# Performance work log

Hardware: AMD Instinct MI355X
Metric: run time of the kernel (lower is better)

## Reference

```python
import jax, jax.numpy as jnp
import numpy as np

N, F_IN, F_OUT = 8192, 512, 256


def setup_inputs() -> dict:
    key = jax.random.key(0)
    k1, k2, k3, k4 = jax.random.split(key, 4)
    x = jax.random.normal(k1, (N, F_IN), dtype=jnp.float32)
    adj = jax.random.randint(k2, (N, N), 0, 2, dtype=jnp.int32)
    # xavier_uniform with gain=1.414
    limW = 1.414 * np.sqrt(6.0 / (F_IN + F_OUT))
    W = jax.random.uniform(k3, (F_IN, F_OUT), dtype=jnp.float32, minval=-limW, maxval=limW)
    lima = 1.414 * np.sqrt(6.0 / (2 * F_OUT + 1))
    a = jax.random.uniform(k4, (2 * F_OUT, 1), dtype=jnp.float32, minval=-lima, maxval=lima)
    return {"x": x, "adj": adj, "W": W, "a": a}


def reference(x, adj, W, a):
    # h = x @ W : [N, F_out]
    h = x @ W
    f_out = h.shape[1]
    # additive score a^T [h_i ; h_j] is separable: (h @ a_l)_i + (h @ a_r)_j
    f_src = h @ a[:f_out, 0]   # [N]
    f_dst = h @ a[f_out:, 0]   # [N]
    e = jax.nn.leaky_relu(f_src[:, None] + f_dst[None, :], negative_slope=0.2)  # [N, N]
    e = jnp.where(adj > 0, e, jnp.float32(-9e15))
    attention = jax.nn.softmax(e, axis=1)  # row-wise over neighbors
    # dropout(p=0.6) is identity in eval mode
    h_prime = attention @ h  # [N, F_out]
    return h_prime
```

## Files before the change

kernel.cpp:

```cpp
#include <hip/hip_runtime.h>
#include <hip/hip_bf16.h>

#define NN 8192
#define FIN 512
#define FOUT 256
#define JTILE 64

typedef __attribute__((ext_vector_type(8))) short short8;
typedef __attribute__((ext_vector_type(4))) short short4v;
typedef __attribute__((ext_vector_type(4))) float float4v;
typedef __attribute__((ext_vector_type(16))) float float16v;

__device__ __forceinline__ short f2bf(float f) {
    union { float f; unsigned u; } v; v.f = f;
    unsigned r = (v.u + 0x7FFFu + ((v.u >> 16) & 1u)) >> 16;
    return (short)r;
}

__global__ __launch_bounds__(256) void wt_kernel(const float* __restrict__ W,
                                                 short* __restrict__ Wt) {
    __shared__ short tile[32][33];
    int tx = threadIdx.x & 31, ty = threadIdx.x >> 5;
    int k0 = blockIdx.x * 32, n0 = blockIdx.y * 32;
#pragma unroll
    for (int r = 0; r < 32; r += 8)
        tile[ty + r][tx] = f2bf(W[(size_t)(k0 + ty + r) * FOUT + n0 + tx]);
    __syncthreads();
#pragma unroll
    for (int r = 0; r < 32; r += 8)
        Wt[(size_t)(n0 + ty + r) * FIN + k0 + tx] = tile[tx][ty + r];
}

__global__ __launch_bounds__(256) void h_kernel(const float* __restrict__ x,
                                                const short* __restrict__ Wt,
                                                const float* __restrict__ a,
                                                short* __restrict__ h_t,
                                                float* __restrict__ f_src,
                                                float* __restrict__ f_dst) {
    int wave = (blockIdx.x << 2) + (threadIdx.x >> 6);
    int lane = threadIdx.x & 63;
    int m0 = (wave & 511) << 4;
    int n0 = (wave >> 9) << 6;
    int lr = lane & 15, lq = lane >> 4;

    const float* xrow = x + (size_t)(m0 + lr) * FIN + lq * 8;
    const short* wbase = Wt + (size_t)(n0 + lr) * FIN + lq * 8;

    float4v acc[4] = {};
    for (int k0 = 0; k0 < FIN; k0 += 32) {
        float4v xa = *(const float4v*)(xrow + k0);
        float4v xb = *(const float4v*)(xrow + k0 + 4);
        short8 av;
        av[0] = f2bf(xa[0]); av[1] = f2bf(xa[1]); av[2] = f2bf(xa[2]); av[3] = f2bf(xa[3]);
        av[4] = f2bf(xb[0]); av[5] = f2bf(xb[1]); av[6] = f2bf(xb[2]); av[7] = f2bf(xb[3]);
#pragma unroll
        for (int ct = 0; ct < 4; ct++) {
            short8 bv = *(const short8*)(wbase + (size_t)ct * 16 * FIN + k0);
            acc[ct] = __builtin_amdgcn_mfma_f32_16x16x32_bf16(av, bv, acc[ct], 0, 0, 0);
        }
    }
    float s_part[4] = {0.f, 0.f, 0.f, 0.f};
    float d_part[4] = {0.f, 0.f, 0.f, 0.f};
#pragma unroll
    for (int ct = 0; ct < 4; ct++) {
        int n = n0 + ct * 16 + lr;
        float al = a[n], ar = a[FOUT + n];
#pragma unroll
        for (int reg = 0; reg < 4; reg++) {
            float hv = acc[ct][reg];
            s_part[reg] = fmaf(hv, al, s_part[reg]);
            d_part[reg] = fmaf(hv, ar, d_part[reg]);
            h_t[(size_t)n * NN + (m0 + lq * 4 + reg)] = f2bf(hv);
        }
    }
#pragma unroll
    for (int off = 1; off < 16; off <<= 1) {
#pragma unroll
        for (int reg = 0; reg < 4; reg++) {
            s_part[reg] += __shfl_xor(s_part[reg], off);
            d_part[reg] += __shfl_xor(d_part[reg], off);
        }
    }
    const float LOG2E = 1.4426950408889634f;
    if (lr == 0) {
#pragma unroll
        for (int reg = 0; reg < 4; reg++) {
            atomicAdd(&f_src[m0 + lq * 4 + reg], s_part[reg] * LOG2E);
            atomicAdd(&f_dst[m0 + lq * 4 + reg], d_part[reg] * LOG2E);
        }
    }
}

__global__ __launch_bounds__(256, 2) void gat_kernel(const int* __restrict__ adj,
                                                     const short* __restrict__ h_t,
                                                     const float* __restrict__ f_src,
                                                     const float* __restrict__ f_dst,
                                                     float* __restrict__ Opart,
                                                     float* __restrict__ lpart,
                                                     int jlen) {
    __shared__ short Ht[256 * 72];
    __shared__ short Pt[64 * 72];
    __shared__ float Fd[2][64];

    const int t = threadIdx.x;
    const int i0 = blockIdx.x * 64;
    const int slice = blockIdx.y;
    const int jbase = slice * jlen;

    const int prow = t >> 2, pjq = t & 3;
    const int lane = t & 63, w = t >> 6;
    const int l31 = lane & 31, lq = lane >> 5;
    const int wn0 = w * 64;

    const float fs = f_src[i0 + prow];
    const int* adjRow = adj + (size_t)(i0 + prow) * NN;
    const short* hrow = h_t + ((size_t)t << 13);

    float16v acc00 = {}, acc01 = {}, acc10 = {}, acc11 = {};
    float lp = 0.f;

    if (t < 16) *(float4*)&Fd[0][t * 4] = *(const float4*)(f_dst + jbase + t * 4);
    int4 av0 = *(const int4*)(adjRow + jbase + pjq * 16);
    int4 av1 = *(const int4*)(adjRow + jbase + pjq * 16 + 4);
    int4 av2 = *(const int4*)(adjRow + jbase + pjq * 16 + 8);
    int4 av3 = *(const int4*)(adjRow + jbase + pjq * 16 + 12);
    __syncthreads();

    int buf = 0;
    for (int jo = 0; jo < jlen; jo += JTILE) {
        const int j0 = jbase + jo;
        {
            const float* fdc = &Fd[buf][pjq * 16];
            short8 pbl, pbh;
            int4 avs[4] = {av0, av1, av2, av3};
#pragma unroll
            for (int g = 0; g < 4; g++) {
                const int* ai = (const int*)&avs[g];
#pragma unroll
                for (int q = 0; q < 4; q++) {
                    float y = fs + fdc[g * 4 + q];
                    y = fmaxf(y, 0.2f * y);
                    float e = exp2f(y);
                    float p = (ai[q] != 0) ? e : 0.f;
                    lp += p;
                    short pb = f2bf(p);
                    if (g < 2) pbl[g * 4 + q] = pb; else pbh[(g - 2) * 4 + q] = pb;
                }
            }
            *(short8*)&Pt[prow * 72 + pjq * 16] = pbl;
            *(short8*)&Pt[prow * 72 + pjq * 16 + 8] = pbh;
        }
#pragma unroll
        for (int q = 0; q < 8; q++)
            *(short8*)&Ht[t * 72 + q * 8] = *(const short8*)(hrow + j0 + q * 8);

        if (jo + JTILE < jlen) {
            if (t < 16) *(float4*)&Fd[buf ^ 1][t * 4] = *(const float4*)(f_dst + j0 + JTILE + t * 4);
            av0 = *(const int4*)(adjRow + j0 + JTILE + pjq * 16);
            av1 = *(const int4*)(adjRow + j0 + JTILE + pjq * 16 + 4);
            av2 = *(const int4*)(adjRow + j0 + JTILE + pjq * 16 + 8);
            av3 = *(const int4*)(adjRow + j0 + JTILE + pjq * 16 + 12);
        }
        __syncthreads();

#pragma unroll
        for (int kk = 0; kk < 4; kk++) {
            short8 a0 = *(const short8*)&Pt[l31 * 72 + kk * 16 + lq * 8];
            short8 a1 = *(const short8*)&Pt[(32 + l31) * 72 + kk * 16 + lq * 8];
            short8 b0 = *(const short8*)&Ht[(wn0 + l31) * 72 + kk * 16 + lq * 8];
            short8 b1 = *(const short8*)&Ht[(wn0 + 32 + l31) * 72 + kk * 16 + lq * 8];
            acc00 = __builtin_amdgcn_mfma_f32_32x32x16_bf16(a0, b0, acc00, 0, 0, 0);
            acc01 = __builtin_amdgcn_mfma_f32_32x32x16_bf16(a0, b1, acc01, 0, 0, 0);
            acc10 = __builtin_amdgcn_mfma_f32_32x32x16_bf16(a1, b0, acc10, 0, 0, 0);
            acc11 = __builtin_amdgcn_mfma_f32_32x32x16_bf16(a1, b1, acc11, 0, 0, 0);
        }
        buf ^= 1;
        __syncthreads();
    }

    lp += __shfl_xor(lp, 1);
    lp += __shfl_xor(lp, 2);
    if (pjq == 0) lpart[slice * NN + i0 + prow] = lp;

    float* obase = Opart + ((size_t)slice * NN + i0) * FOUT;
#pragma unroll
    for (int rt = 0; rt < 2; rt++) {
#pragma unroll
        for (int nt = 0; nt < 2; nt++) {
            const float16v& av = rt == 0 ? (nt == 0 ? acc00 : acc01) : (nt == 0 ? acc10 : acc11);
#pragma unroll
            for (int reg = 0; reg < 16; reg++) {
                int row = rt * 32 + (reg & 3) + 8 * (reg >> 2) + 4 * lq;
                int n = wn0 + nt * 32 + l31;
                obase[(size_t)row * FOUT + n] = av[reg];
            }
        }
    }
}

__global__ __launch_bounds__(256) void combine_kernel(const float* __restrict__ Opart,
                                                      const float* __restrict__ lpart,
                                                      float* __restrict__ out, int slices) {
    int i = blockIdx.x, n = threadIdx.x;
    float o = 0.f, l = 0.f;
    for (int s = 0; s < slices; s++) {
        o += Opart[((size_t)s * NN + i) * FOUT + n];
        l += lpart[s * NN + i];
    }
    out[(size_t)i * FOUT + n] = o / l;
}

extern "C" void kernel_launch(void* const* d_in, const int* in_sizes, int n_in,
                              void* d_out, int out_size, void* d_ws, size_t ws_size,
                              hipStream_t stream) {
    const float* x   = (const float*)d_in[0];
    const int*   adj = (const int*)d_in[1];
    const float* W   = (const float*)d_in[2];
    const float* a   = (const float*)d_in[3];
    float* out = (float*)d_out;

    char* ws = (char*)d_ws;
    short* h_t   = (short*)ws;
    short* Wt    = (short*)(ws + (4u << 20));
    float* f_src = (float*)(ws + (4u << 20) + (256u << 10));
    float* f_dst = (float*)(ws + (4u << 20) + (288u << 10));
    float* lpart = (float*)(ws + (4u << 20) + (320u << 10));
    float* Opart = (float*)(ws + (5u << 20));

    const size_t OSLICE = (size_t)NN * FOUT * 4;
    int slices = 1;
    if (ws_size >= (5u << 20) + 4 * OSLICE) slices = 4;
    else if (ws_size >= (5u << 20) + 2 * OSLICE) slices = 2;
    int jlen = NN / slices;

    hipMemsetAsync(f_src, 0, 2 * NN * sizeof(float), stream);
    wt_kernel<<<dim3(FIN / 32, FOUT / 32), 256, 0, stream>>>(W, Wt);
    h_kernel<<<512, 256, 0, stream>>>(x, Wt, a, h_t, f_src, f_dst);
    gat_kernel<<<dim3(NN / 64, slices), 256, 0, stream>>>(adj, h_t, f_src, f_dst,
                                                          Opart, lpart, jlen);
    combine_kernel<<<NN, 256, 0, stream>>>(Opart, lpart, out, slices);
}
```

Before: 448.1 us.

## Restructure GAT kernel: register-resident P fragments, 128-row tiles, swizzled double-buffered H

Each wave now computes its attention probabilities straight into MFMA A-operand registers for its own 32 rows, so the shared-memory P tile and one barrier per tile go away. The row tile doubles to 128, so each staged H chunk is reused by twice as many rows. H is double-buffered in XOR-swizzled LDS with global loads interleaved between MFMA steps, and the adjacency and f_dst values are prefetched two steps ahead. The split-K slice count rises to 8 when workspace allows, which costs more partial-output traffic in the combine step and raises register pressure from 8 accumulators per wave.

```diff
diff --git a/kernel.cpp b/kernel.cpp
--- a/kernel.cpp
+++ b/kernel.cpp
@@ -4,10 +4,8 @@
 #define NN 8192
 #define FIN 512
 #define FOUT 256
-#define JTILE 64
 
 typedef __attribute__((ext_vector_type(8))) short short8;
-typedef __attribute__((ext_vector_type(4))) short short4v;
 typedef __attribute__((ext_vector_type(4))) float float4v;
 typedef __attribute__((ext_vector_type(16))) float float16v;
 
@@ -98,102 +96,127 @@
                                                      float* __restrict__ Opart,
                                                      float* __restrict__ lpart,
                                                      int jlen) {
-    __shared__ short Ht[256 * 72];
-    __shared__ short Pt[64 * 72];
-    __shared__ float Fd[2][64];
+    __shared__ short Bb[2][256 * 64];
 
     const int t = threadIdx.x;
-    const int i0 = blockIdx.x * 64;
+    const int lane = t & 63;
+    const int w = t >> 6;
+    const int l31 = lane & 31, lq = lane >> 5;
+    const int i0 = blockIdx.x * 128;
     const int slice = blockIdx.y;
     const int jbase = slice * jlen;
-
-    const int prow = t >> 2, pjq = t & 3;
-    const int lane = t & 63, w = t >> 6;
-    const int l31 = lane & 31, lq = lane >> 5;
-    const int wn0 = w * 64;
-
-    const float fs = f_src[i0 + prow];
-    const int* adjRow = adj + (size_t)(i0 + prow) * NN;
-    const short* hrow = h_t + ((size_t)t << 13);
-
-    float16v acc00 = {}, acc01 = {}, acc10 = {}, acc11 = {};
+    const int myrow = i0 + w * 32 + l31;
+    const int rsw = l31 & 7;
+    const int swz = t & 7;
+    const int nchunk = jlen >> 6;
+
+    const float fs = f_src[myrow];
+    const int* adjL = adj + (size_t)myrow * NN + jbase + lq * 8;
+    const float* fdL = f_dst + jbase + lq * 8;
+    const short* hrow = h_t + (size_t)t * NN + jbase;
+
+    float16v acc[8] = {};
     float lp = 0.f;
 
-    if (t < 16) *(float4*)&Fd[0][t * 4] = *(const float4*)(f_dst + jbase + t * 4);
-    int4 av0 = *(const int4*)(adjRow + jbase + pjq * 16);
-    int4 av1 = *(const int4*)(adjRow + jbase + pjq * 16 + 4);
-    int4 av2 = *(const int4*)(adjRow + jbase + pjq * 16 + 8);
-    int4 av3 = *(const int4*)(adjRow + jbase + pjq * 16 + 12);
+    int4 aj[2][2];
+    float4 fd[2][2];
+    aj[0][0] = *(const int4*)(adjL);       aj[0][1] = *(const int4*)(adjL + 4);
+    fd[0][0] = *(const float4*)(fdL);      fd[0][1] = *(const float4*)(fdL + 4);
+    aj[1][0] = *(const int4*)(adjL + 16);  aj[1][1] = *(const int4*)(adjL + 20);
+    fd[1][0] = *(const float4*)(fdL + 16); fd[1][1] = *(const float4*)(fdL + 20);
+
+    {
+#pragma unroll
+        for (int q = 0; q < 8; q++) {
+            short8 b = *(const short8*)(hrow + q * 8);
+            *(short8*)(&Bb[0][0] + t * 64 + ((q ^ swz) << 3)) = b;
+        }
+    }
     __syncthreads();
 
-    int buf = 0;
-    for (int jo = 0; jo < jlen; jo += JTILE) {
-        const int j0 = jbase + jo;
-        {
-            const float* fdc = &Fd[buf][pjq * 16];
-            short8 pbl, pbh;
-            int4 avs[4] = {av0, av1, av2, av3};
-#pragma unroll
-            for (int g = 0; g < 4; g++) {
-                const int* ai = (const int*)&avs[g];
-#pragma unroll
-                for (int q = 0; q < 4; q++) {
-                    float y = fs + fdc[g * 4 + q];
-                    y = fmaxf(y, 0.2f * y);
-                    float e = exp2f(y);
-                    float p = (ai[q] != 0) ? e : 0.f;
-                    lp += p;
-                    short pb = f2bf(p);
-                    if (g < 2) pbl[g * 4 + q] = pb; else pbh[(g - 2) * 4 + q] = pb;
-                }
+    for (int c = 0; c < nchunk; ++c) {
+        short* curb = &Bb[c & 1][0];
+        short* nxtb = &Bb[(c & 1) ^ 1][0];
+        const int jn = (c + 1 < nchunk) ? (c + 1) * 64 : 0;
+
+        auto kstep = [&](int kk) {
+            const int s = kk & 1;
+            const int4 A0 = aj[s][0], A1 = aj[s][1];
+            const float4 F0 = fd[s][0], F1 = fd[s][1];
+            int off = (c * 4 + kk + 2) * 16;
+            if (off >= jlen) off -= jlen;
+            aj[s][0] = *(const int4*)(adjL + off);
+            aj[s][1] = *(const int4*)(adjL + off + 4);
+            fd[s][0] = *(const float4*)(fdL + off);
+            fd[s][1] = *(const float4*)(fdL + off + 4);
+
+            const int* ai0 = (const int*)&A0;
+            const int* ai1 = (const int*)&A1;
+            const float* ff0 = (const float*)&F0;
+            const float* ff1 = (const float*)&F1;
+            short8 af;
+#pragma unroll
+            for (int q = 0; q < 4; q++) {
+                float y = fs + ff0[q];
+                y = fmaxf(y, 0.2f * y);
+                float e = exp2f(y);
+                float p = ai0[q] ? e : 0.f;
+                lp += p;
+                af[q] = f2bf(p);
             }
-            *(short8*)&Pt[prow * 72 + pjq * 16] = pbl;
-            *(short8*)&Pt[prow * 72 + pjq * 16 + 8] = pbh;
-        }
-#pragma unroll
-        for (int q = 0; q < 8; q++)
-            *(short8*)&Ht[t * 72 + q * 8] = *(const short8*)(hrow + j0 + q * 8);
-
-        if (jo + JTILE < jlen) {
-            if (t < 16) *(float4*)&Fd[buf ^ 1][t * 4] = *(const float4*)(f_dst + j0 + JTILE + t * 4);
-            av0 = *(const int4*)(adjRow + j0 + JTILE + pjq * 16);
-            av1 = *(const int4*)(adjRow + j0 + JTILE + pjq * 16 + 4);
-            av2 = *(const int4*)(adjRow + j0 + JTILE + pjq * 16 + 8);
-            av3 = *(const int4*)(adjRow + j0 + JTILE + pjq * 16 + 12);
-        }
-        __syncthreads();
-
-#pragma unroll
-        for (int kk = 0; kk < 4; kk++) {
-            short8 a0 = *(const short8*)&Pt[l31 * 72 + kk * 16 + lq * 8];
-            short8 a1 = *(const short8*)&Pt[(32 + l31) * 72 + kk * 16 + lq * 8];
-            short8 b0 = *(const short8*)&Ht[(wn0 + l31) * 72 + kk * 16 + lq * 8];
-            short8 b1 = *(const short8*)&Ht[(wn0 + 32 + l31) * 72 + kk * 16 + lq * 8];
-            acc00 = __builtin_amdgcn_mfma_f32_32x32x16_bf16(a0, b0, acc00, 0, 0, 0);
-            acc01 = __builtin_amdgcn_mfma_f32_32x32x16_bf16(a0, b1, acc01, 0, 0, 0);
-            acc10 = __builtin_amdgcn_mfma_f32_32x32x16_bf16(a1, b0, acc10, 0, 0, 0);
-            acc11 = __builtin_amdgcn_mfma_f32_32x32x16_bf16(a1, b1, acc11, 0, 0, 0);
-        }
-        buf ^= 1;
-        __syncthreads();
-    }
-
-    lp += __shfl_xor(lp, 1);
-    lp += __shfl_xor(lp, 2);
-    if (pjq == 0) lpart[slice * NN + i0 + prow] = lp;
-
-    float* obase = Opart + ((size_t)slice * NN + i0) * FOUT;
-#pragma unroll
-    for (int rt = 0; rt < 2; rt++) {
-#pragma unroll
-        for (int nt = 0; nt < 2; nt++) {
-            const float16v& av = rt == 0 ? (nt == 0 ? acc00 : acc01) : (nt == 0 ? acc10 : acc11);
-#pragma unroll
-            for (int reg = 0; reg < 16; reg++) {
-                int row = rt * 32 + (reg & 3) + 8 * (reg >> 2) + 4 * lq;
-                int n = wn0 + nt * 32 + l31;
-                obase[(size_t)row * FOUT + n] = av[reg];
+#pragma unroll
+            for (int q = 0; q < 4; q++) {
+                float y = fs + ff1[q];
+                y = fmaxf(y, 0.2f * y);
+                float e = exp2f(y);
+                float p = ai1[q] ? e : 0.f;
+                lp += p;
+                af[4 + q] = f2bf(p);
             }
+            const int cb = ((kk * 2 + lq) ^ rsw) << 3;
+#pragma unroll
+            for (int nt = 0; nt < 8; nt++) {
+                short8 b = *(const short8*)(curb + (nt * 32 + l31) * 64 + cb);
+                acc[nt] = __builtin_amdgcn_mfma_f32_32x32x16_bf16(af, b, acc[nt], 0, 0, 0);
+            }
+        };
+
+        short8 s0 = *(const short8*)(hrow + jn + 0);
+        short8 s1 = *(const short8*)(hrow + jn + 8);
+        short8 s2 = *(const short8*)(hrow + jn + 16);
+        short8 s3 = *(const short8*)(hrow + jn + 24);
+        kstep(0);
+        kstep(1);
+        *(short8*)(nxtb + t * 64 + ((0 ^ swz) << 3)) = s0;
+        *(short8*)(nxtb + t * 64 + ((1 ^ swz) << 3)) = s1;
+        *(short8*)(nxtb + t * 64 + ((2 ^ swz) << 3)) = s2;
+        *(short8*)(nxtb + t * 64 + ((3 ^ swz) << 3)) = s3;
+        short8 s4 = *(const short8*)(hrow + jn + 32);
+        short8 s5 = *(const short8*)(hrow + jn + 40);
+        short8 s6 = *(const short8*)(hrow + jn + 48);
+        short8 s7 = *(const short8*)(hrow + jn + 56);
+        kstep(2);
+        kstep(3);
+        *(short8*)(nxtb + t * 64 + ((4 ^ swz) << 3)) = s4;
+        *(short8*)(nxtb + t * 64 + ((5 ^ swz) << 3)) = s5;
+        *(short8*)(nxtb + t * 64 + ((6 ^ swz) << 3)) = s6;
+        *(short8*)(nxtb + t * 64 + ((7 ^ swz) << 3)) = s7;
+
+        asm volatile("s_waitcnt lgkmcnt(0)" ::: "memory");
+        asm volatile("s_barrier" ::: "memory");
+    }
+
+    lp += __shfl_xor(lp, 32);
+    if (lq == 0) lpart[(size_t)slice * NN + myrow] = lp;
+
+    float* ob = Opart + ((size_t)slice * NN + i0 + w * 32) * FOUT;
+#pragma unroll
+    for (int nt = 0; nt < 8; nt++) {
+        int n = nt * 32 + l31;
+#pragma unroll
+        for (int reg = 0; reg < 16; reg++) {
+            int row = (reg & 3) + 8 * (reg >> 2) + 4 * lq;
+            ob[(size_t)row * FOUT + n] = acc[nt][reg];
         }
     }
 }
@@ -205,7 +228,7 @@
     float o = 0.f, l = 0.f;
     for (int s = 0; s < slices; s++) {
         o += Opart[((size_t)s * NN + i) * FOUT + n];
-        l += lpart[s * NN + i];
+        l += lpart[(size_t)s * NN + i];
     }
     out[(size_t)i * FOUT + n] = o / l;
 }
@@ -225,18 +248,18 @@
     float* f_src = (float*)(ws + (4u << 20) + (256u << 10));
     float* f_dst = (float*)(ws + (4u << 20) + (288u << 10));
     float* lpart = (float*)(ws + (4u << 20) + (320u << 10));
-    float* Opart = (float*)(ws + (5u << 20));
+    float* Opart = (float*)(ws + (8u << 20));
 
     const size_t OSLICE = (size_t)NN * FOUT * 4;
-    int slices = 1;
-    if (ws_size >= (5u << 20) + 4 * OSLICE) slices = 4;
-    else if (ws_size >= (5u << 20) + 2 * OSLICE) slices = 2;
+    int slices = 2;
+    if (ws_size >= (8u << 20) + 8 * OSLICE) slices = 8;
+    else if (ws_size >= (8u << 20) + 4 * OSLICE) slices = 4;
     int jlen = NN / slices;
 
     hipMemsetAsync(f_src, 0, 2 * NN * sizeof(float), stream);
     wt_kernel<<<dim3(FIN / 32, FOUT / 32), 256, 0, stream>>>(W, Wt);
     h_kernel<<<512, 256, 0, stream>>>(x, Wt, a, h_t, f_src, f_dst);
-    gat_kernel<<<dim3(NN / 64, slices), 256, 0, stream>>>(adj, h_t, f_src, f_dst,
-                                                          Opart, lpart, jlen);
+    gat_kernel<<<dim3(NN / 128, slices), 256, 0, stream>>>(adj, h_t, f_src, f_dst,
+                                                           Opart, lpart, jlen);
     combine_kernel<<<NN, 256, 0, stream>>>(Opart, lpart, out, slices);
 }
```

Result: slower. 474.7 us (+5.9%).
